# Performance work log

Measured on AMD Instinct MI355X. Metric: run time of the kernel, lower is better.

The kernel has to match this reference:

```python
import jax, jax.numpy as jnp
import numpy as np

FOCUS = 3.0
EPS = 1e-6


def setup_inputs() -> dict:
    key = jax.random.key(0)
    ks = jax.random.split(key, 8)
    C, h = 768, 12
    d = C // h
    H = W = T = 16
    l = 4
    Nx = H * W * T * l
    Nm = H * W * T
    B = 2

    def w(k, sh, s=0.02):
        return jax.random.normal(k, sh, jnp.float32) * s

    return {
        "x": jax.random.normal(ks[0], (Nx, B, C), jnp.float32),
        "memory": jax.random.normal(ks[1], (Nm, B, C), jnp.float32),
        "w_q": w(ks[2], (C, C)),
        "w_k": w(ks[3], (C, C)),
        "w_v": w(ks[4], (C, C)),
        "w_proj": w(ks[5], (C, C)),
        "b_proj": jnp.zeros((C,), jnp.float32),
        "dwc_w": w(ks[6], (d, 1, 5, 5)),
        "dwc_b": jnp.zeros((d,), jnp.float32),
        "scale": w(ks[7], (1, 1, C)),
        "H": H, "W": W, "T": T, "l": l,
    }


def _process(t, scale_sp):
    # focusing feature map: relu, rescale, elementwise power, renormalize to original norm
    t = jax.nn.relu(t) + EPS
    t = t / scale_sp
    n = jnp.linalg.norm(t, axis=-1, keepdims=True)
    tp = t ** FOCUS
    return tp / jnp.linalg.norm(tp, axis=-1, keepdims=True) * n


def _dwconv(v5, w, b):
    # depthwise conv2d, kernel 5, pad 2; v5: (B*h, d, H, W*T), w: (d,1,5,5)
    out = jax.lax.conv_general_dilated(
        v5, w, window_strides=(1, 1), padding=((2, 2), (2, 2)),
        dimension_numbers=("NCHW", "OIHW", "NCHW"),
        feature_group_count=v5.shape[1])
    return out + b[None, :, None, None]


def reference(x, memory, w_q, w_k, w_v, w_proj, b_proj, dwc_w, dwc_b, scale, H, W, T, l):
    x = x.transpose(1, 0, 2)          # (B, Nx, C)
    memory = memory.transpose(1, 0, 2)  # (B, Nm, C)
    B, Nx, C = x.shape
    Nm = memory.shape[1]
    d = dwc_w.shape[0]
    h = C // d

    q = jnp.einsum("bnc,dc->bnd", x, w_q)
    k = jnp.einsum("bnc,dc->bnd", memory, w_k)
    v = jnp.einsum("bnc,dc->bnd", memory, w_v)

    scale_sp = jax.nn.softplus(scale)
    q = _process(q, scale_sp)
    k = _process(k, scale_sp)

    q = q.reshape(B, Nx, h, d).transpose(0, 2, 1, 3)  # (B,h,Nx,d)
    k = k.reshape(B, Nm, h, d).transpose(0, 2, 1, 3)  # (B,h,Nm,d)
    v = v.reshape(B, Nm, h, d).transpose(0, 2, 1, 3)  # (B,h,Nm,d)

    k_mean = k.mean(axis=2, keepdims=True)            # (B,h,1,d)
    z = 1.0 / (jnp.einsum("bhnd,bhmd->bhnm", q, k_mean) + EPS)  # (B,h,Nx,1)

    inv = float(Nm) ** -0.5
    kv = jnp.einsum("bhnd,bhne->bhde", k * inv, v * inv)        # (B,h,d,d)
    out = jnp.einsum("bhnd,bhde->bhne", q, kv) * z              # (B,h,Nx,d)
    out = out.transpose(0, 2, 1, 3).reshape(B, Nx, C)

    # depthwise conv enhancement on v over (H, W*T) grid
    v5 = v.reshape(B * h, H, W, T, d).transpose(0, 4, 1, 2, 3).reshape(B * h, d, H, W * T)
    dwc = _dwconv(v5, dwc_w, dwc_b)                   # (B*h, d, H, W*T)
    dwc = dwc.reshape(B, C, Nm).transpose(0, 2, 1)    # (B, Nm, C)
    out = out + jnp.tile(dwc, (1, l, 1))              # (B, Nx, C)

    out = jnp.einsum("bnc,dc->bnd", out, w_proj) + b_proj
    return out.transpose(1, 0, 2)                     # (Nx, B, C)
```

## Files before the change

kernel.cpp:

```cpp
#include <hip/hip_runtime.h>

#define CD 768
#define NHEAD 12
#define DH 64
#define BSZ 2
#define NM_ 4096
#define NX_ 16384
#define EPSF 1e-6f
#define KSTR 1536

using bf16x8 = __attribute__((ext_vector_type(8))) short;
using f32x4  = __attribute__((ext_vector_type(4))) float;

__device__ inline unsigned short bf16r(float f) {
  union { float f; unsigned u; } un; un.f = f;
  unsigned u = un.u;
  u += 0x7fffu + ((u >> 16) & 1u);
  return (unsigned short)(u >> 16);
}
__device__ inline float b2f(unsigned short u) {
  union { unsigned u; float f; } x; x.u = ((unsigned)u) << 16; return x.f;
}
__device__ inline float asf(unsigned u) {
  union { unsigned u; float f; } x; x.u = u; return x.f;
}
__device__ inline void gl2lds16(const void* g, void* l) {
  __builtin_amdgcn_global_load_lds(
      (const __attribute__((address_space(1))) void*)g,
      (__attribute__((address_space(3))) void*)l, 16, 0, 0);
}

__global__ __launch_bounds__(256) void cvt_bf16(const float* __restrict__ in,
                                                unsigned short* __restrict__ out, int n4) {
  int i = blockIdx.x * 256 + threadIdx.x;
  if (i >= n4) return;
  float4 v = ((const float4*)in)[i];
  ushort4 o;
  o.x = bf16r(v.x); o.y = bf16r(v.y); o.z = bf16r(v.z); o.w = bf16r(v.w);
  ((ushort4*)out)[i] = o;
}

__global__ void softplus_k(const float* __restrict__ s, float* __restrict__ sp) {
  int i = blockIdx.x * 256 + threadIdx.x;
  if (i < CD) sp[i] = log1pf(expf(s[i]));
}

template<int OUTBF>
__global__ __launch_bounds__(256) void gemm128(const unsigned short* __restrict__ A,
                                               const unsigned short* __restrict__ B,
                                               void* __restrict__ Cv,
                                               const float* __restrict__ bias,
                                               int M, int N, int K) {
  __shared__ __align__(16) unsigned short As[128 * 32];
  __shared__ __align__(16) unsigned short Bs[128 * 32];
  const int m0 = blockIdx.x * 128, n0 = blockIdx.y * 128;
  const int tid = threadIdx.x, wave = tid >> 6, lane = tid & 63;
  const int quad = lane >> 4, l16 = lane & 15;
  const int wm = (wave >> 1) * 64, wn = (wave & 1) * 64;
  const int srow = lane >> 2, scol = (lane & 3) * 8;
  f32x4 acc[4][4] = {};
  for (int k0 = 0; k0 < K; k0 += 32) {
    __syncthreads();
    #pragma unroll
    for (int c2 = 0; c2 < 2; ++c2) {
      int ch = wave * 2 + c2;
      gl2lds16(A + (size_t)(m0 + ch * 16 + srow) * K + k0 + scol, (void*)(As + ch * 512));
      gl2lds16(B + (size_t)(n0 + ch * 16 + srow) * K + k0 + scol, (void*)(Bs + ch * 512));
    }
    __syncthreads();
    bf16x8 a[4], bb[4];
    #pragma unroll
    for (int t = 0; t < 4; ++t) {
      a[t]  = *(const bf16x8*)(As + (wm + t * 16 + l16) * 32 + quad * 8);
      bb[t] = *(const bf16x8*)(Bs + (wn + t * 16 + l16) * 32 + quad * 8);
    }
    #pragma unroll
    for (int tm = 0; tm < 4; ++tm)
      #pragma unroll
      for (int tn = 0; tn < 4; ++tn)
        acc[tm][tn] = __builtin_amdgcn_mfma_f32_16x16x32_bf16(a[tm], bb[tn], acc[tm][tn], 0, 0, 0);
  }
  #pragma unroll
  for (int tm = 0; tm < 4; ++tm)
    #pragma unroll
    for (int tn = 0; tn < 4; ++tn) {
      const int col = n0 + wn + tn * 16 + l16;
      const float bv = bias ? bias[col] : 0.f;
      #pragma unroll
      for (int r = 0; r < 4; ++r) {
        const int row = m0 + wm + tm * 16 + quad * 4 + r;
        float v = acc[tm][tn][r] + bv;
        if (OUTBF) ((unsigned short*)Cv)[(size_t)row * N + col] = bf16r(v);
        else       ((float*)Cv)[(size_t)row * N + col] = v;
      }
    }
}

__global__ __launch_bounds__(256) void process_rows(float* __restrict__ X,
                                                    const float* __restrict__ sp) {
  const int row = blockIdx.x;
  const int tid = threadIdx.x;
  float* xr = X + (size_t)row * CD;
  float tv[3];
  float n2 = 0.f, m2 = 0.f;
  #pragma unroll
  for (int i = 0; i < 3; ++i) {
    int c = tid + i * 256;
    float t = fmaxf(xr[c], 0.f) + EPSF;
    t = t / sp[c];
    tv[i] = t;
    float t2 = t * t;
    n2 += t2;
    float p = t2 * t;
    m2 += p * p;
  }
  #pragma unroll
  for (int off = 32; off; off >>= 1) {
    n2 += __shfl_down(n2, off, 64);
    m2 += __shfl_down(m2, off, 64);
  }
  __shared__ float rn[4], rm[4];
  if ((tid & 63) == 0) { rn[tid >> 6] = n2; rm[tid >> 6] = m2; }
  __syncthreads();
  float N2 = rn[0] + rn[1] + rn[2] + rn[3];
  float M2 = rm[0] + rm[1] + rm[2] + rm[3];
  float factor = sqrtf(N2 / M2);
  unsigned short* xo = (unsigned short*)xr;
  #pragma unroll
  for (int i = 0; i < 3; ++i) {
    int c = tid + i * 256;
    float t = tv[i];
    xo[c] = bf16r(t * t * t * factor);
  }
}

__global__ __launch_bounds__(256) void kmean_k(const unsigned short* __restrict__ Kp,
                                               float* __restrict__ km) {
  int blk = blockIdx.x;
  int b = blk / 48;
  int r = blk % 48;
  int cch = r / 16, nch = r % 16;
  int c = cch * 256 + threadIdx.x;
  float s = 0.f;
  for (int i = 0; i < 256; ++i) {
    int n = nch * 256 + i;
    s += b2f(Kp[((size_t)n * BSZ + b) * KSTR + c]);
  }
  atomicAdd(&km[b * CD + c], s * (1.f / NM_));
}

__global__ __launch_bounds__(256) void kv_k(const unsigned short* __restrict__ Kp,
                                            const unsigned short* __restrict__ Vp,
                                            float* __restrict__ kv) {
  const int bh = blockIdx.x;
  const int b = bh / NHEAD, hh = bh % NHEAD;
  const int nch = blockIdx.y;
  __shared__ float ks[64][68];
  __shared__ float vs[64][68];
  const int tid = threadIdx.x;
  const int d = tid & 63, eg = tid >> 6;
  const int rn = tid >> 2, cb = (tid & 3) * 16;
  float acc[16];
  #pragma unroll
  for (int j = 0; j < 16; ++j) acc[j] = 0.f;
  for (int sub = 0; sub < 4; ++sub) {
    int n0 = nch * 256 + sub * 64;
    __syncthreads();
    const unsigned short* kg = Kp + ((size_t)(n0 + rn) * BSZ + b) * KSTR + hh * 64 + cb;
    const unsigned short* vg = Vp + ((size_t)(n0 + rn) * BSZ + b) * CD + hh * 64 + cb;
    #pragma unroll
    for (int i = 0; i < 4; ++i) {
      ushort4 k4 = *(const ushort4*)(kg + i * 4);
      ushort4 v4 = *(const ushort4*)(vg + i * 4);
      ks[rn][cb + i * 4 + 0] = b2f(k4.x); ks[rn][cb + i * 4 + 1] = b2f(k4.y);
      ks[rn][cb + i * 4 + 2] = b2f(k4.z); ks[rn][cb + i * 4 + 3] = b2f(k4.w);
      vs[rn][cb + i * 4 + 0] = b2f(v4.x); vs[rn][cb + i * 4 + 1] = b2f(v4.y);
      vs[rn][cb + i * 4 + 2] = b2f(v4.z); vs[rn][cb + i * 4 + 3] = b2f(v4.w);
    }
    __syncthreads();
    for (int n = 0; n < 64; ++n) {
      float a = ks[n][d];
      const float* vr = &vs[n][eg * 16];
      #pragma unroll
      for (int j = 0; j < 16; ++j) acc[j] += a * vr[j];
    }
  }
  float* outp = kv + (size_t)bh * 4096 + d * 64 + eg * 16;
  #pragma unroll
  for (int j = 0; j < 16; ++j) atomicAdd(&outp[j], acc[j] * (1.f / NM_));
}

__global__ __launch_bounds__(256) void cvt_kvT(const float* __restrict__ kv,
                                               unsigned short* __restrict__ kvT) {
  int idx = blockIdx.x * 256 + threadIdx.x;
  if (idx >= BSZ * NHEAD * 4096) return;
  int bh = idx >> 12, r = idx & 4095;
  int e = r >> 6, d = r & 63;
  kvT[(size_t)bh * 4096 + (size_t)e * 64 + d] = bf16r(kv[(size_t)bh * 4096 + (size_t)d * 64 + e]);
}

__global__ __launch_bounds__(256) void dwconv_k(const unsigned short* __restrict__ Vp,
                                                const float* __restrict__ w,
                                                const float* __restrict__ bias,
                                                unsigned short* __restrict__ outp) {
  __shared__ __align__(16) unsigned ls32[16 * 20 * 32];
  __shared__ float wsm[64 * 25];
  __shared__ float bsm[64];
  const int tid = threadIdx.x;
  const int bh = blockIdx.x, b = bh / NHEAD, h = bh % NHEAD;
  const int x0 = blockIdx.y * 16;
  for (int i = tid; i < 1600; i += 256) wsm[i] = w[i];
  if (tid < 64) bsm[tid] = bias[tid];
  const int lch = (tid & 7) * 8;
  #pragma unroll
  for (int it = 0; it < 10; ++it) {
    int p = it * 32 + (tid >> 3);
    int y = p / 20, xp = p % 20;
    int xx = x0 + xp - 2;
    int4 val = {0, 0, 0, 0};
    if (xx >= 0 && xx < 256)
      val = *(const int4*)(Vp + ((size_t)((y << 8) + xx) * BSZ + b) * CD + h * 64 + lch);
    *(int4*)((unsigned short*)ls32 + p * 64 + lch) = val;
  }
  __syncthreads();
  const int cp = tid & 31;
  const int xs = tid >> 5;
  float wr0[25], wr1[25];
  #pragma unroll
  for (int t = 0; t < 25; ++t) { wr0[t] = wsm[(cp * 2) * 25 + t]; wr1[t] = wsm[(cp * 2 + 1) * 25 + t]; }
  const float b0 = bsm[cp * 2], b1 = bsm[cp * 2 + 1];
  for (int y = 0; y < 16; ++y) {
    float a00 = b0, a01 = b1, a10 = b0, a11 = b1;
    #pragma unroll
    for (int dy = 0; dy < 5; ++dy) {
      int yy = y + dy - 2;
      if (yy < 0 || yy >= 16) continue;
      #pragma unroll
      for (int dx = 0; dx < 5; ++dx) {
        int base = (yy * 20 + xs * 2 + dx) * 32 + cp;
        unsigned u0 = ls32[base], u1 = ls32[base + 32];
        float w0 = wr0[dy * 5 + dx], w1 = wr1[dy * 5 + dx];
        a00 += w0 * asf(u0 << 16);  a01 += w1 * asf(u0 & 0xffff0000u);
        a10 += w0 * asf(u1 << 16);  a11 += w1 * asf(u1 & 0xffff0000u);
      }
    }
    const int x = x0 + xs * 2;
    size_t o = ((size_t)((y << 8) + x) * BSZ + b) * CD + h * 64 + cp * 2;
    ushort2 s0; s0.x = bf16r(a00); s0.y = bf16r(a01);
    ushort2 s1; s1.x = bf16r(a10); s1.y = bf16r(a11);
    *(ushort2*)(outp + o) = s0;
    *(ushort2*)(outp + o + (size_t)BSZ * CD) = s1;
  }
}

__global__ __launch_bounds__(256) void attn_mfma(const unsigned short* __restrict__ Qb,
                                                 const unsigned short* __restrict__ kvT,
                                                 const float* __restrict__ km,
                                                 const unsigned short* __restrict__ dwcb,
                                                 unsigned short* __restrict__ tmpb) {
  __shared__ __align__(16) unsigned short qs[128 * 64];
  __shared__ __align__(16) unsigned short kvs[64 * 64];
  __shared__ float kms[64];
  __shared__ float zs[128];
  const int bh = blockIdx.x, b = bh / NHEAD, h = bh % NHEAD;
  const int n0 = blockIdx.y * 128;
  const int tid = threadIdx.x, wave = tid >> 6, lane = tid & 63;
  const int quad = lane >> 4, l16 = lane & 15;
  #pragma unroll
  for (int c2 = 0; c2 < 4; ++c2) {
    int ch = wave * 4 + c2;
    int row = ch * 8 + (lane >> 3);
    int col = (lane & 7) * 8;
    gl2lds16(Qb + ((size_t)(n0 + row) * BSZ + b) * KSTR + h * 64 + col, (void*)(qs + ch * 512));
  }
  #pragma unroll
  for (int c2 = 0; c2 < 2; ++c2) {
    int ch = wave * 2 + c2;
    int e = ch * 8 + (lane >> 3);
    int col = (lane & 7) * 8;
    gl2lds16(kvT + (size_t)bh * 4096 + e * 64 + col, (void*)(kvs + ch * 512));
  }
  if (tid < 64) kms[tid] = km[b * CD + h * 64 + tid];
  __syncthreads();
  if (tid < 128) {
    float s = 0.f;
    for (int d2 = 0; d2 < 64; ++d2) s += b2f(qs[tid * 64 + d2]) * kms[d2];
    zs[tid] = 1.f / (s + EPSF);
  }
  __syncthreads();
  f32x4 acc[2][4] = {};
  #pragma unroll
  for (int kh = 0; kh < 2; ++kh) {
    bf16x8 a0 = *(const bf16x8*)(qs + (wave * 32 + l16) * 64 + kh * 32 + quad * 8);
    bf16x8 a1 = *(const bf16x8*)(qs + (wave * 32 + 16 + l16) * 64 + kh * 32 + quad * 8);
    bf16x8 bt[4];
    #pragma unroll
    for (int tn = 0; tn < 4; ++tn)
      bt[tn] = *(const bf16x8*)(kvs + (tn * 16 + l16) * 64 + kh * 32 + quad * 8);
    #pragma unroll
    for (int tn = 0; tn < 4; ++tn) {
      acc[0][tn] = __builtin_amdgcn_mfma_f32_16x16x32_bf16(a0, bt[tn], acc[0][tn], 0, 0, 0);
      acc[1][tn] = __builtin_amdgcn_mfma_f32_16x16x32_bf16(a1, bt[tn], acc[1][tn], 0, 0, 0);
    }
  }
  #pragma unroll
  for (int tm = 0; tm < 2; ++tm)
    #pragma unroll
    for (int tn = 0; tn < 4; ++tn)
      #pragma unroll
      for (int r = 0; r < 4; ++r) {
        int rl = wave * 32 + tm * 16 + quad * 4 + r;
        int n = n0 + rl;
        int m = n & (NM_ - 1);
        int c = h * 64 + tn * 16 + l16;
        float val = acc[tm][tn][r] * zs[rl] + b2f(dwcb[((size_t)m * BSZ + b) * CD + c]);
        tmpb[((size_t)n * BSZ + b) * CD + c] = bf16r(val);
      }
}

extern "C" void kernel_launch(void* const* d_in, const int* in_sizes, int n_in,
                              void* d_out, int out_size, void* d_ws, size_t ws_size,
                              hipStream_t stream) {
  const float* x      = (const float*)d_in[0];
  const float* memory = (const float*)d_in[1];
  const float* w_q    = (const float*)d_in[2];
  const float* w_k    = (const float*)d_in[3];
  const float* w_v    = (const float*)d_in[4];
  const float* w_proj = (const float*)d_in[5];
  const float* b_proj = (const float*)d_in[6];
  const float* dwc_w  = (const float*)d_in[7];
  const float* dwc_b  = (const float*)d_in[8];
  const float* scale  = (const float*)d_in[9];
  float* out = (float*)d_out;

  const int Mq = NX_ * BSZ;
  const int Mm = NM_ * BSZ;

  char* ws = (char*)d_ws;
  size_t off = 0;
  auto alloc = [&](size_t bytes) -> void* {
    void* p = ws + off;
    off += (bytes + 255) & ~(size_t)255;
    return p;
  };
  float* q    = (float*)alloc((size_t)Mq * CD * 4);
  float* kbuf = (float*)alloc((size_t)Mm * CD * 4);
  float* kv   = (float*)alloc((size_t)BSZ * NHEAD * DH * DH * 4);
  float* km   = (float*)alloc((size_t)BSZ * CD * 4);
  float* sp   = (float*)alloc(CD * 4);
  unsigned short* xb   = (unsigned short*)alloc((size_t)Mq * CD * 2);
  unsigned short* mb   = (unsigned short*)alloc((size_t)Mm * CD * 2);
  unsigned short* vb   = (unsigned short*)alloc((size_t)Mm * CD * 2);
  unsigned short* dwcb = (unsigned short*)alloc((size_t)Mm * CD * 2);
  unsigned short* kvT  = (unsigned short*)alloc((size_t)BSZ * NHEAD * DH * DH * 2);
  unsigned short* wqb  = (unsigned short*)alloc((size_t)CD * CD * 2);
  unsigned short* wkb  = (unsigned short*)alloc((size_t)CD * CD * 2);
  unsigned short* wvb  = (unsigned short*)alloc((size_t)CD * CD * 2);
  unsigned short* wpb  = (unsigned short*)alloc((size_t)CD * CD * 2);

  hipMemsetAsync(kv, 0, (size_t)BSZ * NHEAD * DH * DH * 4, stream);
  hipMemsetAsync(km, 0, (size_t)BSZ * CD * 4, stream);

  softplus_k<<<3, 256, 0, stream>>>(scale, sp);

  auto cvt = [&](const float* src, unsigned short* dst, size_t n) {
    int n4 = (int)(n / 4);
    cvt_bf16<<<(n4 + 255) / 256, 256, 0, stream>>>(src, dst, n4);
  };
  cvt(x,      xb,  (size_t)Mq * CD);
  cvt(memory, mb,  (size_t)Mm * CD);
  cvt(w_q,    wqb, (size_t)CD * CD);
  cvt(w_k,    wkb, (size_t)CD * CD);
  cvt(w_v,    wvb, (size_t)CD * CD);
  cvt(w_proj, wpb, (size_t)CD * CD);

  gemm128<0><<<dim3(Mq / 128, CD / 128), 256, 0, stream>>>(xb, wqb, q,    nullptr, Mq, CD, CD);
  gemm128<0><<<dim3(Mm / 128, CD / 128), 256, 0, stream>>>(mb, wkb, kbuf, nullptr, Mm, CD, CD);
  gemm128<1><<<dim3(Mm / 128, CD / 128), 256, 0, stream>>>(mb, wvb, vb,   nullptr, Mm, CD, CD);

  process_rows<<<Mq, 256, 0, stream>>>(q, sp);
  process_rows<<<Mm, 256, 0, stream>>>(kbuf, sp);

  const unsigned short* qb = (const unsigned short*)q;
  const unsigned short* kb = (const unsigned short*)kbuf;

  kmean_k<<<96, 256, 0, stream>>>(kb, km);
  kv_k<<<dim3(BSZ * NHEAD, 16), 256, 0, stream>>>(kb, vb, kv);
  cvt_kvT<<<(BSZ * NHEAD * 4096 + 255) / 256, 256, 0, stream>>>(kv, kvT);

  dwconv_k<<<dim3(BSZ * NHEAD, 16), 256, 0, stream>>>(vb, dwc_w, dwc_b, dwcb);

  unsigned short* tmpb = xb;
  attn_mfma<<<dim3(BSZ * NHEAD, NX_ / 128), 256, 0, stream>>>(qb, kvT, km, dwcb, tmpb);

  gemm128<0><<<dim3(Mq / 128, CD / 128), 256, 0, stream>>>(tmpb, wpb, out, b_proj, Mq, CD, CD);
}
```

Before: 606.6 us.

## Fuse fp32-to-bf16 input conversion into GEMM loads and restructure KV reduction

The projection GEMMs now read fp32 activations directly, convert them to bf16 in registers and store them to LDS, which removes the separate conversion passes over x and memory. The weight conversions and softplus are merged into one prep kernel. The atomic-based kv and k-mean kernels plus the transpose kernel are replaced by a per-chunk partial-sum kernel and a deterministic reduce kernel that also writes the transposed bf16 kv. The trade-off is that the A-operand loads now go through registers instead of direct global-to-LDS loads, and the GEMMs read twice the bytes for A.

```diff
diff --git a/kernel.cpp b/kernel.cpp
--- a/kernel.cpp
+++ b/kernel.cpp
@@ -8,6 +8,7 @@
 #define NX_ 16384
 #define EPSF 1e-6f
 #define KSTR 1536
+#define KVCH 32
 
 using bf16x8 = __attribute__((ext_vector_type(8))) short;
 using f32x4  = __attribute__((ext_vector_type(4))) float;
@@ -30,23 +31,29 @@
       (__attribute__((address_space(3))) void*)l, 16, 0, 0);
 }
 
-__global__ __launch_bounds__(256) void cvt_bf16(const float* __restrict__ in,
-                                                unsigned short* __restrict__ out, int n4) {
-  int i = blockIdx.x * 256 + threadIdx.x;
-  if (i >= n4) return;
-  float4 v = ((const float4*)in)[i];
-  ushort4 o;
-  o.x = bf16r(v.x); o.y = bf16r(v.y); o.z = bf16r(v.z); o.w = bf16r(v.w);
-  ((ushort4*)out)[i] = o;
-}
-
-__global__ void softplus_k(const float* __restrict__ s, float* __restrict__ sp) {
-  int i = blockIdx.x * 256 + threadIdx.x;
-  if (i < CD) sp[i] = log1pf(expf(s[i]));
-}
-
-template<int OUTBF>
-__global__ __launch_bounds__(256) void gemm128(const unsigned short* __restrict__ A,
+__global__ __launch_bounds__(256) void prep_k(const float* __restrict__ w0, const float* __restrict__ w1,
+                                              const float* __restrict__ w2, const float* __restrict__ w3,
+                                              const float* __restrict__ scale,
+                                              unsigned short* __restrict__ o0, unsigned short* __restrict__ o1,
+                                              unsigned short* __restrict__ o2, unsigned short* __restrict__ o3,
+                                              float* __restrict__ sp) {
+  int bx = blockIdx.x;
+  if (bx < 2304) {
+    int m = bx / 576;
+    int i = (bx % 576) * 256 + threadIdx.x;
+    const float* w = m == 0 ? w0 : m == 1 ? w1 : m == 2 ? w2 : w3;
+    unsigned short* o = m == 0 ? o0 : m == 1 ? o1 : m == 2 ? o2 : o3;
+    float4 v = ((const float4*)w)[i];
+    ushort4 u; u.x = bf16r(v.x); u.y = bf16r(v.y); u.z = bf16r(v.z); u.w = bf16r(v.w);
+    ((ushort4*)o)[i] = u;
+  } else {
+    int i = (bx - 2304) * 256 + threadIdx.x;
+    if (i < CD) sp[i] = log1pf(expf(scale[i]));
+  }
+}
+
+template<int AFP32, int OUTBF>
+__global__ __launch_bounds__(256) void gemm128(const void* __restrict__ Av,
                                                const unsigned short* __restrict__ B,
                                                void* __restrict__ Cv,
                                                const float* __restrict__ bias,
@@ -58,13 +65,39 @@
   const int quad = lane >> 4, l16 = lane & 15;
   const int wm = (wave >> 1) * 64, wn = (wave & 1) * 64;
   const int srow = lane >> 2, scol = (lane & 3) * 8;
+  const int ar = tid >> 2, ac = (tid & 3) * 8;
   f32x4 acc[4][4] = {};
   for (int k0 = 0; k0 < K; k0 += 32) {
+    float4 f0, f1, f2, f3;
+    if (AFP32) {
+      const float* Af = (const float*)Av;
+      f0 = *(const float4*)(Af + (size_t)(m0 + ar) * K + k0 + ac);
+      f1 = *(const float4*)(Af + (size_t)(m0 + ar) * K + k0 + ac + 4);
+      f2 = *(const float4*)(Af + (size_t)(m0 + ar + 64) * K + k0 + ac);
+      f3 = *(const float4*)(Af + (size_t)(m0 + ar + 64) * K + k0 + ac + 4);
+    }
     __syncthreads();
+    if (AFP32) {
+      ushort4 u0, u1, u2, u3;
+      u0.x = bf16r(f0.x); u0.y = bf16r(f0.y); u0.z = bf16r(f0.z); u0.w = bf16r(f0.w);
+      u1.x = bf16r(f1.x); u1.y = bf16r(f1.y); u1.z = bf16r(f1.z); u1.w = bf16r(f1.w);
+      u2.x = bf16r(f2.x); u2.y = bf16r(f2.y); u2.z = bf16r(f2.z); u2.w = bf16r(f2.w);
+      u3.x = bf16r(f3.x); u3.y = bf16r(f3.y); u3.z = bf16r(f3.z); u3.w = bf16r(f3.w);
+      *(ushort4*)(As + ar * 32 + ac) = u0;
+      *(ushort4*)(As + ar * 32 + ac + 4) = u1;
+      *(ushort4*)(As + (ar + 64) * 32 + ac) = u2;
+      *(ushort4*)(As + (ar + 64) * 32 + ac + 4) = u3;
+    } else {
+      const unsigned short* A = (const unsigned short*)Av;
+      #pragma unroll
+      for (int c2 = 0; c2 < 2; ++c2) {
+        int ch = wave * 2 + c2;
+        gl2lds16(A + (size_t)(m0 + ch * 16 + srow) * K + k0 + scol, (void*)(As + ch * 512));
+      }
+    }
     #pragma unroll
     for (int c2 = 0; c2 < 2; ++c2) {
       int ch = wave * 2 + c2;
-      gl2lds16(A + (size_t)(m0 + ch * 16 + srow) * K + k0 + scol, (void*)(As + ch * 512));
       gl2lds16(B + (size_t)(n0 + ch * 16 + srow) * K + k0 + scol, (void*)(Bs + ch * 512));
     }
     __syncthreads();
@@ -134,69 +167,92 @@
   }
 }
 
-__global__ __launch_bounds__(256) void kmean_k(const unsigned short* __restrict__ Kp,
-                                               float* __restrict__ km) {
-  int blk = blockIdx.x;
-  int b = blk / 48;
-  int r = blk % 48;
-  int cch = r / 16, nch = r % 16;
-  int c = cch * 256 + threadIdx.x;
-  float s = 0.f;
-  for (int i = 0; i < 256; ++i) {
-    int n = nch * 256 + i;
-    s += b2f(Kp[((size_t)n * BSZ + b) * KSTR + c]);
-  }
-  atomicAdd(&km[b * CD + c], s * (1.f / NM_));
-}
-
-__global__ __launch_bounds__(256) void kv_k(const unsigned short* __restrict__ Kp,
-                                            const unsigned short* __restrict__ Vp,
-                                            float* __restrict__ kv) {
-  const int bh = blockIdx.x;
-  const int b = bh / NHEAD, hh = bh % NHEAD;
-  const int nch = blockIdx.y;
-  __shared__ float ks[64][68];
-  __shared__ float vs[64][68];
+__global__ __launch_bounds__(256) void kv_part_k(const unsigned short* __restrict__ Kp,
+                                                 const unsigned short* __restrict__ Vp,
+                                                 float* __restrict__ kvp,
+                                                 float* __restrict__ kmp) {
+  const int bh = blockIdx.x, chunk = blockIdx.y;
+  const int b = bh / NHEAD, h = bh % NHEAD;
+  const int n0 = chunk * 128;
+  __shared__ __align__(16) unsigned short ks[128 * 72];
+  __shared__ __align__(16) unsigned short vs[128 * 72];
   const int tid = threadIdx.x;
-  const int d = tid & 63, eg = tid >> 6;
-  const int rn = tid >> 2, cb = (tid & 3) * 16;
-  float acc[16];
-  #pragma unroll
-  for (int j = 0; j < 16; ++j) acc[j] = 0.f;
-  for (int sub = 0; sub < 4; ++sub) {
-    int n0 = nch * 256 + sub * 64;
+  #pragma unroll
+  for (int it = 0; it < 4; ++it) {
+    int g = it * 256 + tid;
+    int row = g >> 3, c8 = (g & 7) * 8;
+    int4 ka = *(const int4*)(Kp + ((size_t)(n0 + row) * BSZ + b) * KSTR + h * 64 + c8);
+    int4 va = *(const int4*)(Vp + ((size_t)(n0 + row) * BSZ + b) * CD + h * 64 + c8);
+    *(int4*)(ks + row * 72 + c8) = ka;
+    *(int4*)(vs + row * 72 + c8) = va;
+  }
+  __syncthreads();
+  const int d0 = (tid >> 4) * 4, e0 = (tid & 15) * 4;
+  float acc[4][4] = {};
+  #pragma unroll 4
+  for (int n = 0; n < 128; ++n) {
+    ushort4 kd = *(const ushort4*)(ks + n * 72 + d0);
+    ushort4 ve = *(const ushort4*)(vs + n * 72 + e0);
+    float kf[4] = {b2f(kd.x), b2f(kd.y), b2f(kd.z), b2f(kd.w)};
+    float vf[4] = {b2f(ve.x), b2f(ve.y), b2f(ve.z), b2f(ve.w)};
+    #pragma unroll
+    for (int i = 0; i < 4; ++i)
+      #pragma unroll
+      for (int j = 0; j < 4; ++j) acc[i][j] += kf[i] * vf[j];
+  }
+  float* outp = kvp + ((size_t)chunk * 24 + bh) * 4096;
+  #pragma unroll
+  for (int i = 0; i < 4; ++i) {
+    float4 o; o.x = acc[i][0]; o.y = acc[i][1]; o.z = acc[i][2]; o.w = acc[i][3];
+    *(float4*)(outp + (d0 + i) * 64 + e0) = o;
+  }
+  if (tid < 64) {
+    float s = 0.f;
+    for (int n = 0; n < 128; ++n) s += b2f(ks[n * 72 + tid]);
+    kmp[((size_t)chunk * 24 + bh) * 64 + tid] = s;
+  }
+}
+
+__global__ __launch_bounds__(256) void kv_reduce_k(const float* __restrict__ kvp,
+                                                   const float* __restrict__ kmp,
+                                                   unsigned short* __restrict__ kvT,
+                                                   float* __restrict__ km) {
+  const int tid = threadIdx.x;
+  const int bx = blockIdx.x;
+  if (bx < 24) {
+    __shared__ float t[64 * 65];
+    float acc[16] = {};
+    const float* base = kvp + (size_t)bx * 4096 + tid * 16;
+    for (int c = 0; c < KVCH; ++c) {
+      const float* p = base + (size_t)c * 24 * 4096;
+      #pragma unroll
+      for (int i = 0; i < 4; ++i) {
+        float4 v = *(const float4*)(p + i * 4);
+        acc[i * 4 + 0] += v.x; acc[i * 4 + 1] += v.y; acc[i * 4 + 2] += v.z; acc[i * 4 + 3] += v.w;
+      }
+    }
+    const int d = tid >> 2, e0 = (tid & 3) * 16;
+    #pragma unroll
+    for (int i = 0; i < 16; ++i) t[d * 65 + e0 + i] = acc[i] * (1.f / NM_);
     __syncthreads();
-    const unsigned short* kg = Kp + ((size_t)(n0 + rn) * BSZ + b) * KSTR + hh * 64 + cb;
-    const unsigned short* vg = Vp + ((size_t)(n0 + rn) * BSZ + b) * CD + hh * 64 + cb;
-    #pragma unroll
-    for (int i = 0; i < 4; ++i) {
-      ushort4 k4 = *(const ushort4*)(kg + i * 4);
-      ushort4 v4 = *(const ushort4*)(vg + i * 4);
-      ks[rn][cb + i * 4 + 0] = b2f(k4.x); ks[rn][cb + i * 4 + 1] = b2f(k4.y);
-      ks[rn][cb + i * 4 + 2] = b2f(k4.z); ks[rn][cb + i * 4 + 3] = b2f(k4.w);
-      vs[rn][cb + i * 4 + 0] = b2f(v4.x); vs[rn][cb + i * 4 + 1] = b2f(v4.y);
-      vs[rn][cb + i * 4 + 2] = b2f(v4.z); vs[rn][cb + i * 4 + 3] = b2f(v4.w);
-    }
-    __syncthreads();
-    for (int n = 0; n < 64; ++n) {
-      float a = ks[n][d];
-      const float* vr = &vs[n][eg * 16];
-      #pragma unroll
-      for (int j = 0; j < 16; ++j) acc[j] += a * vr[j];
-    }
-  }
-  float* outp = kv + (size_t)bh * 4096 + d * 64 + eg * 16;
-  #pragma unroll
-  for (int j = 0; j < 16; ++j) atomicAdd(&outp[j], acc[j] * (1.f / NM_));
-}
-
-__global__ __launch_bounds__(256) void cvt_kvT(const float* __restrict__ kv,
-                                               unsigned short* __restrict__ kvT) {
-  int idx = blockIdx.x * 256 + threadIdx.x;
-  if (idx >= BSZ * NHEAD * 4096) return;
-  int bh = idx >> 12, r = idx & 4095;
-  int e = r >> 6, d = r & 63;
-  kvT[(size_t)bh * 4096 + (size_t)e * 64 + d] = bf16r(kv[(size_t)bh * 4096 + (size_t)d * 64 + e]);
+    const int e = tid >> 2, dd0 = (tid & 3) * 16;
+    ushort4 o[4];
+    #pragma unroll
+    for (int i = 0; i < 16; ++i)
+      ((unsigned short*)o)[i] = bf16r(t[(dd0 + i) * 65 + e]);
+    unsigned short* dst = kvT + (size_t)bx * 4096 + e * 64 + dd0;
+    *(ushort4*)(dst) = o[0]; *(ushort4*)(dst + 4) = o[1];
+    *(ushort4*)(dst + 8) = o[2]; *(ushort4*)(dst + 12) = o[3];
+  } else {
+    int i = (bx - 24) * 256 + tid;
+    if (i < 24 * 64) {
+      int bhh = i >> 6, d = i & 63;
+      float s = 0.f;
+      for (int c = 0; c < KVCH; ++c) s += kmp[((size_t)c * 24 + bhh) * 64 + d];
+      int b = bhh / NHEAD, h = bhh % NHEAD;
+      km[b * CD + h * 64 + d] = s * (1.f / NM_);
+    }
+  }
 }
 
 __global__ __launch_bounds__(256) void dwconv_k(const unsigned short* __restrict__ Vp,
@@ -345,11 +401,11 @@
   };
   float* q    = (float*)alloc((size_t)Mq * CD * 4);
   float* kbuf = (float*)alloc((size_t)Mm * CD * 4);
-  float* kv   = (float*)alloc((size_t)BSZ * NHEAD * DH * DH * 4);
+  float* kvp  = (float*)alloc((size_t)KVCH * 24 * 4096 * 4);
+  float* kmp  = (float*)alloc((size_t)KVCH * 24 * 64 * 4);
   float* km   = (float*)alloc((size_t)BSZ * CD * 4);
   float* sp   = (float*)alloc(CD * 4);
-  unsigned short* xb   = (unsigned short*)alloc((size_t)Mq * CD * 2);
-  unsigned short* mb   = (unsigned short*)alloc((size_t)Mm * CD * 2);
+  unsigned short* tmpb = (unsigned short*)alloc((size_t)Mq * CD * 2);
   unsigned short* vb   = (unsigned short*)alloc((size_t)Mm * CD * 2);
   unsigned short* dwcb = (unsigned short*)alloc((size_t)Mm * CD * 2);
   unsigned short* kvT  = (unsigned short*)alloc((size_t)BSZ * NHEAD * DH * DH * 2);
@@ -358,25 +414,11 @@
   unsigned short* wvb  = (unsigned short*)alloc((size_t)CD * CD * 2);
   unsigned short* wpb  = (unsigned short*)alloc((size_t)CD * CD * 2);
 
-  hipMemsetAsync(kv, 0, (size_t)BSZ * NHEAD * DH * DH * 4, stream);
-  hipMemsetAsync(km, 0, (size_t)BSZ * CD * 4, stream);
-
-  softplus_k<<<3, 256, 0, stream>>>(scale, sp);
-
-  auto cvt = [&](const float* src, unsigned short* dst, size_t n) {
-    int n4 = (int)(n / 4);
-    cvt_bf16<<<(n4 + 255) / 256, 256, 0, stream>>>(src, dst, n4);
-  };
-  cvt(x,      xb,  (size_t)Mq * CD);
-  cvt(memory, mb,  (size_t)Mm * CD);
-  cvt(w_q,    wqb, (size_t)CD * CD);
-  cvt(w_k,    wkb, (size_t)CD * CD);
-  cvt(w_v,    wvb, (size_t)CD * CD);
-  cvt(w_proj, wpb, (size_t)CD * CD);
-
-  gemm128<0><<<dim3(Mq / 128, CD / 128), 256, 0, stream>>>(xb, wqb, q,    nullptr, Mq, CD, CD);
-  gemm128<0><<<dim3(Mm / 128, CD / 128), 256, 0, stream>>>(mb, wkb, kbuf, nullptr, Mm, CD, CD);
-  gemm128<1><<<dim3(Mm / 128, CD / 128), 256, 0, stream>>>(mb, wvb, vb,   nullptr, Mm, CD, CD);
+  prep_k<<<2307, 256, 0, stream>>>(w_q, w_k, w_v, w_proj, scale, wqb, wkb, wvb, wpb, sp);
+
+  gemm128<1, 0><<<dim3(Mq / 128, CD / 128), 256, 0, stream>>>(x,      wqb, q,    nullptr, Mq, CD, CD);
+  gemm128<1, 0><<<dim3(Mm / 128, CD / 128), 256, 0, stream>>>(memory, wkb, kbuf, nullptr, Mm, CD, CD);
+  gemm128<1, 1><<<dim3(Mm / 128, CD / 128), 256, 0, stream>>>(memory, wvb, vb,   nullptr, Mm, CD, CD);
 
   process_rows<<<Mq, 256, 0, stream>>>(q, sp);
   process_rows<<<Mm, 256, 0, stream>>>(kbuf, sp);
@@ -384,14 +426,12 @@
   const unsigned short* qb = (const unsigned short*)q;
   const unsigned short* kb = (const unsigned short*)kbuf;
 
-  kmean_k<<<96, 256, 0, stream>>>(kb, km);
-  kv_k<<<dim3(BSZ * NHEAD, 16), 256, 0, stream>>>(kb, vb, kv);
-  cvt_kvT<<<(BSZ * NHEAD * 4096 + 255) / 256, 256, 0, stream>>>(kv, kvT);
+  kv_part_k<<<dim3(24, KVCH), 256, 0, stream>>>(kb, vb, kvp, kmp);
+  kv_reduce_k<<<30, 256, 0, stream>>>(kvp, kmp, kvT, km);
 
   dwconv_k<<<dim3(BSZ * NHEAD, 16), 256, 0, stream>>>(vb, dwc_w, dwc_b, dwcb);
 
-  unsigned short* tmpb = xb;
   attn_mfma<<<dim3(BSZ * NHEAD, NX_ / 128), 256, 0, stream>>>(qb, kvT, km, dwcb, tmpb);
 
-  gemm128<0><<<dim3(Mq / 128, CD / 128), 256, 0, stream>>>(tmpb, wpb, out, b_proj, Mq, CD, CD);
-}
+  gemm128<0, 0><<<dim3(Mq / 128, CD / 128), 256, 0, stream>>>(tmpb, wpb, out, b_proj, Mq, CD, CD);
+}
```

Measured after the change: 517.8 us. 14.6% less time.
